# Performance work log

Measured on AMD Instinct MI355X. Metric: run time of the kernel, lower is better.

The kernel has to match this reference:

```python
import jax, jax.numpy as jnp
import numpy as np

N_NODES = 50000
N_EDGES = 800000
IN_DIM = 128
HID_DIM = 256
OUT_DIM = 5
BATCH = 50000  # batch_size in module; view(batch_size, 5)


def _sage_conv(x, src, dst, Wl, bl, Wr):
    # PyG SAGEConv (aggr='mean', root_weight=True, normalize=False):
    #   out = lin_l(mean_{j in N(i)} x_j) + lin_r(x_i)
    msgs = x[src]                                            # [E, d]
    agg = jax.ops.segment_sum(msgs, dst, num_segments=N_NODES)
    cnt = jax.ops.segment_sum(jnp.ones((src.shape[0],), x.dtype), dst,
                              num_segments=N_NODES)          # [N]
    mean = agg / jnp.maximum(cnt, 1.0)[:, None]              # 0 for isolated nodes
    return mean @ Wl.T + bl + x @ Wr.T


def setup_inputs() -> dict:
    key = jax.random.key(0)
    ks = jax.random.split(key, 8)
    x = jax.random.normal(ks[0], (N_NODES, IN_DIM), dtype=jnp.float32)
    edge_index = jax.random.randint(ks[1], (2, N_EDGES), 0, N_NODES, dtype=jnp.int64)
    s1 = 1.0 / np.sqrt(IN_DIM)
    s2 = 1.0 / np.sqrt(HID_DIM)
    W1l = jax.random.uniform(ks[2], (HID_DIM, IN_DIM), jnp.float32, -s1, s1)
    b1l = jax.random.uniform(ks[3], (HID_DIM,), jnp.float32, -s1, s1)
    W1r = jax.random.uniform(ks[4], (HID_DIM, IN_DIM), jnp.float32, -s1, s1)
    W2l = jax.random.uniform(ks[5], (OUT_DIM, HID_DIM), jnp.float32, -s2, s2)
    b2l = jax.random.uniform(ks[6], (OUT_DIM,), jnp.float32, -s2, s2)
    W2r = jax.random.uniform(ks[7], (OUT_DIM, HID_DIM), jnp.float32, -s2, s2)
    return {"x": x, "edge_index": edge_index,
            "W1l": W1l, "b1l": b1l, "W1r": W1r,
            "W2l": W2l, "b2l": b2l, "W2r": W2r}


def reference(x, edge_index, W1l, b1l, W1r, W2l, b2l, W2r):
    src, dst = edge_index[0], edge_index[1]
    h = jax.nn.relu(_sage_conv(x, src, dst, W1l, b1l, W1r))   # [N, hidden]
    h = jax.nn.relu(_sage_conv(h, src, dst, W2l, b2l, W2r))   # [N, out]
    return h.reshape(BATCH, 5)
```

## Files before the change

kernel.cpp:

```cpp
#include <hip/hip_runtime.h>

static constexpr int NN = 50000;
static constexpr int NE = 800000;
static constexpr int D0 = 128;
static constexpr int D1 = 256;
static constexpr int D2 = 5;

static constexpr int BSZ   = 256;
static constexpr int NBUK  = (NN + BSZ - 1) / BSZ;
static constexpr int CAP   = 4800;
static constexpr int CB    = 400;
static constexpr int CHUNK = 2000;

static constexpr int XB = (NN * 32 + 255) / 256;
static constexpr int WB = (D1 * 64) / 256;
static constexpr int PB = 4;

using short8  = __attribute__((ext_vector_type(8))) short;
using floatx4 = __attribute__((ext_vector_type(4))) float;

__device__ __forceinline__ unsigned short f2b(float f) {
  union { float f; unsigned u; } v; v.f = f;
  unsigned r = v.u + 0x7fffu + ((v.u >> 16) & 1u);
  return (unsigned short)(r >> 16);
}
__device__ __forceinline__ float b2f(unsigned short s) {
  union { unsigned u; float f; } v; v.u = ((unsigned)s) << 16;
  return v.f;
}

__global__ __launch_bounds__(256) void k_prepA(
    const float* __restrict__ x, unsigned short* __restrict__ ab,
    const float* __restrict__ W1l, const float* __restrict__ W1r,
    unsigned short* __restrict__ wb, const float* __restrict__ W2l,
    const float* __restrict__ W2r, unsigned short* __restrict__ w2b,
    const int* __restrict__ src, const int* __restrict__ dst,
    int* __restrict__ gcur, uint2* __restrict__ slab) {
  __shared__ int hist[256], bstart[256], gbase[256], hcur[256], sscan[256];
  __shared__ uint2 pairs[CHUNK];
  const int b = blockIdx.x, t = threadIdx.x;
  if (b < CB) {
    const int e0 = b * CHUNK;
    hist[t] = 0;
    __syncthreads();
    for (int j = t; j < CHUNK; j += 256)
      atomicAdd(&hist[dst[e0 + j] >> 8], 1);
    __syncthreads();
    sscan[t] = hist[t];
    __syncthreads();
    for (int dd = 1; dd < 256; dd <<= 1) {
      int u = (t >= dd) ? sscan[t - dd] : 0;
      __syncthreads();
      sscan[t] += u;
      __syncthreads();
    }
    bstart[t] = sscan[t] - hist[t];
    gbase[t] = (t < NBUK && hist[t] > 0) ? atomicAdd(&gcur[t], hist[t]) : 0;
    hcur[t] = 0;
    __syncthreads();
    for (int j = t; j < CHUNK; j += 256) {
      const int s = src[e0 + j], d = dst[e0 + j];
      const int bk = d >> 8;
      const int pos = bstart[bk] + atomicAdd(&hcur[bk], 1);
      pairs[pos] = make_uint2((unsigned)s, (unsigned)d);
    }
    __syncthreads();
    for (int j = t; j < CHUNK; j += 256) {
      const uint2 pr = pairs[j];
      const int bk = (int)pr.y >> 8;
      slab[(size_t)bk * CAP + gbase[bk] + (j - bstart[bk])] = pr;
    }
    return;
  }
  if (b < CB + XB) {
    int idx = (b - CB) * 256 + t;
    if (idx < NN * 32) {
      int node = idx >> 5, cg = idx & 31;
      float4 v = *(const float4*)(x + (size_t)node * D0 + cg * 4);
      ushort4 o;
      o.x = f2b(v.x); o.y = f2b(v.y); o.z = f2b(v.z); o.w = f2b(v.w);
      *(ushort4*)(ab + (size_t)node * 256 + 128 + cg * 4) = o;
    }
    return;
  }
  if (b < CB + XB + WB) {
    int idx = (b - CB - XB) * 256 + t;
    int c = idx >> 6, k = (idx & 63) * 4;
    const float* srcp = (k < 128) ? (W1l + (size_t)c * 128 + k)
                                  : (W1r + (size_t)c * 128 + (k - 128));
    float4 v = *(const float4*)srcp;
    ushort4 o;
    o.x = f2b(v.x); o.y = f2b(v.y); o.z = f2b(v.z); o.w = f2b(v.w);
    *(ushort4*)(wb + (size_t)c * 256 + k) = o;
    return;
  }
  {
    int idx = (b - CB - XB - WB) * 256 + t;
    int n = idx >> 6, k = (idx & 63) * 4;
    float4 v = {0.f, 0.f, 0.f, 0.f};
    if (n < 5) v = *(const float4*)(W2l + (size_t)n * D1 + k);
    else if (n < 10) v = *(const float4*)(W2r + (size_t)(n - 5) * D1 + k);
    ushort4 o;
    o.x = f2b(v.x); o.y = f2b(v.y); o.z = f2b(v.z); o.w = f2b(v.w);
    *(ushort4*)(w2b + (size_t)n * 256 + k) = o;
  }
}

__global__ __launch_bounds__(256) void k_bucketBC(
    const uint2* __restrict__ slab, const int* __restrict__ gcur,
    int* __restrict__ cur, float* __restrict__ inv,
    int* __restrict__ esort) {
  __shared__ int cnt[BSZ], s[BSZ], lcur[BSZ], g[256];
  __shared__ int sorted[CAP];
  const int b = blockIdx.x, t = threadIdx.x;
  const int n0 = b << 8;
  cnt[t] = 0;
  g[t] = (t < NBUK) ? gcur[t] : 0;
  __syncthreads();
  for (int dd = 1; dd < 256; dd <<= 1) {
    int u = (t >= dd) ? g[t - dd] : 0;
    __syncthreads();
    g[t] += u;
    __syncthreads();
  }
  const int bbase = (b == 0) ? 0 : g[b - 1];
  const int cntE = gcur[b];
  const uint2* sp = slab + (size_t)b * CAP;
  for (int j = t; j < cntE; j += 256)
    atomicAdd(&cnt[(int)sp[j].y - n0], 1);
  __syncthreads();
  s[t] = cnt[t];
  __syncthreads();
  for (int dd = 1; dd < BSZ; dd <<= 1) {
    int u = (t >= dd) ? s[t - dd] : 0;
    __syncthreads();
    s[t] += u;
    __syncthreads();
  }
  const int start = bbase + (s[t] - cnt[t]);
  const int node = n0 + t;
  if (node < NN) {
    cur[node] = start;
    inv[node] = 1.0f / (float)max(cnt[t], 1);
  }
  lcur[t] = s[t] - cnt[t];
  if (b == NBUK - 1 && t == 0) cur[NN] = NE;
  __syncthreads();
  for (int j = t; j < cntE; j += 256) {
    const uint2 pr = sp[j];
    const int p = atomicAdd(&lcur[(int)pr.y - n0], 1);
    sorted[p] = (int)pr.x;
  }
  __syncthreads();
  for (int j = t; j < cntE; j += 256)
    esort[bbase + j] = sorted[j];
}

__global__ __launch_bounds__(256) void k_agg1(
    unsigned short* __restrict__ ab, const int* __restrict__ esort,
    const int* __restrict__ cur, const float* __restrict__ inv) {
  const int i = (blockIdx.x * 256 + threadIdx.x) >> 6;
  const int lane = threadIdx.x & 63;
  if (i >= NN) return;
  int e = cur[i];
  const int end = cur[i + 1];
  float a0 = 0.f, b0 = 0.f, a1 = 0.f, b1 = 0.f;
  float a2 = 0.f, b2 = 0.f, a3 = 0.f, b3 = 0.f;
  const unsigned short* xb = ab + 128 + lane * 2;
  while (e < end && (e & 3)) {
    const unsigned v = *(const unsigned*)(xb + (size_t)esort[e] * 256);
    a0 += b2f((unsigned short)v); b0 += b2f((unsigned short)(v >> 16));
    ++e;
  }
  for (; e + 7 < end; e += 8) {
    const int4 s0 = *(const int4*)(esort + e);
    const int4 s1 = *(const int4*)(esort + e + 4);
    const unsigned v0 = *(const unsigned*)(xb + (size_t)s0.x * 256);
    const unsigned v1 = *(const unsigned*)(xb + (size_t)s0.y * 256);
    const unsigned v2 = *(const unsigned*)(xb + (size_t)s0.z * 256);
    const unsigned v3 = *(const unsigned*)(xb + (size_t)s0.w * 256);
    const unsigned v4 = *(const unsigned*)(xb + (size_t)s1.x * 256);
    const unsigned v5 = *(const unsigned*)(xb + (size_t)s1.y * 256);
    const unsigned v6 = *(const unsigned*)(xb + (size_t)s1.z * 256);
    const unsigned v7 = *(const unsigned*)(xb + (size_t)s1.w * 256);
    a0 += b2f((unsigned short)v0); b0 += b2f((unsigned short)(v0 >> 16));
    a1 += b2f((unsigned short)v1); b1 += b2f((unsigned short)(v1 >> 16));
    a2 += b2f((unsigned short)v2); b2 += b2f((unsigned short)(v2 >> 16));
    a3 += b2f((unsigned short)v3); b3 += b2f((unsigned short)(v3 >> 16));
    a0 += b2f((unsigned short)v4); b0 += b2f((unsigned short)(v4 >> 16));
    a1 += b2f((unsigned short)v5); b1 += b2f((unsigned short)(v5 >> 16));
    a2 += b2f((unsigned short)v6); b2 += b2f((unsigned short)(v6 >> 16));
    a3 += b2f((unsigned short)v7); b3 += b2f((unsigned short)(v7 >> 16));
  }
  if (e + 3 < end) {
    const int4 s0 = *(const int4*)(esort + e);
    const unsigned v0 = *(const unsigned*)(xb + (size_t)s0.x * 256);
    const unsigned v1 = *(const unsigned*)(xb + (size_t)s0.y * 256);
    const unsigned v2 = *(const unsigned*)(xb + (size_t)s0.z * 256);
    const unsigned v3 = *(const unsigned*)(xb + (size_t)s0.w * 256);
    a0 += b2f((unsigned short)v0); b0 += b2f((unsigned short)(v0 >> 16));
    a1 += b2f((unsigned short)v1); b1 += b2f((unsigned short)(v1 >> 16));
    a2 += b2f((unsigned short)v2); b2 += b2f((unsigned short)(v2 >> 16));
    a3 += b2f((unsigned short)v3); b3 += b2f((unsigned short)(v3 >> 16));
    e += 4;
  }
  for (; e < end; ++e) {
    const unsigned v = *(const unsigned*)(xb + (size_t)esort[e] * 256);
    a0 += b2f((unsigned short)v); b0 += b2f((unsigned short)(v >> 16));
  }
  const float sc = inv[i];
  const float sa = (a0 + a1) + (a2 + a3);
  const float sb = (b0 + b1) + (b2 + b3);
  const unsigned out =
      ((unsigned)f2b(sb * sc) << 16) | (unsigned)f2b(sa * sc);
  *(unsigned*)(ab + (size_t)i * 256 + lane * 2) = out;
}

__global__ __launch_bounds__(256) void k_gemm1f(
    const unsigned short* __restrict__ ab, const unsigned short* __restrict__ wb,
    const unsigned short* __restrict__ w2b, const float* __restrict__ b1l,
    float* __restrict__ tt, float* __restrict__ rp) {
  __shared__ short sAB[2 * 128 * 72];
  short* sA = sAB;
  short* sB = sAB + 128 * 72;
  const int tid = threadIdx.x;
  const int row0 = blockIdx.y * 128;
  const int hf = blockIdx.x;
  const int col0 = hf * 128;
  const int wave = tid >> 6, lane = tid & 63;
  const int quad = lane >> 4, m16 = lane & 15;
  const int wm = wave & 1, wn = wave >> 1;
  const int lr = tid >> 2;
  const int lk = (tid & 3) * 8;

  floatx4 acc[4][4];
#pragma unroll
  for (int a = 0; a < 4; ++a)
#pragma unroll
    for (int b = 0; b < 4; ++b) acc[a][b] = {0.f, 0.f, 0.f, 0.f};

  const int gr0 = row0 + lr, gr1 = row0 + lr + 64;
  const bool ok0 = gr0 < NN, ok1 = gr1 < NN;
  const unsigned short* aptr0 = ab + (size_t)gr0 * 256 + lk;
  const unsigned short* aptr1 = ab + (size_t)gr1 * 256 + lk;
  const unsigned short* bptr0 = wb + (size_t)(col0 + lr) * 256 + lk;
  const unsigned short* bptr1 = wb + (size_t)(col0 + lr + 64) * 256 + lk;
  short* sA0 = &sA[lr * 72 + lk];
  short* sA1 = &sA[(lr + 64) * 72 + lk];
  short* sB0 = &sB[lr * 72 + lk];
  short* sB1 = &sB[(lr + 64) * 72 + lk];
  const uint4 zz = make_uint4(0, 0, 0, 0);

  uint4 a00 = ok0 ? *(const uint4*)(aptr0) : zz;
  uint4 a01 = ok0 ? *(const uint4*)(aptr0 + 32) : zz;
  uint4 a10 = ok1 ? *(const uint4*)(aptr1) : zz;
  uint4 a11 = ok1 ? *(const uint4*)(aptr1 + 32) : zz;
  uint4 b00 = *(const uint4*)(bptr0);
  uint4 b01 = *(const uint4*)(bptr0 + 32);
  uint4 b10 = *(const uint4*)(bptr1);
  uint4 b11 = *(const uint4*)(bptr1 + 32);

  for (int kk = 0; kk < 256; kk += 64) {
    __syncthreads();
    *(uint4*)sA0 = a00;
    *(uint4*)(sA0 + 32) = a01;
    *(uint4*)sA1 = a10;
    *(uint4*)(sA1 + 32) = a11;
    *(uint4*)sB0 = b00;
    *(uint4*)(sB0 + 32) = b01;
    *(uint4*)sB1 = b10;
    *(uint4*)(sB1 + 32) = b11;
    __syncthreads();
    if (kk < 192) {
      const int kn = kk + 64;
      a00 = ok0 ? *(const uint4*)(aptr0 + kn) : zz;
      a01 = ok0 ? *(const uint4*)(aptr0 + kn + 32) : zz;
      a10 = ok1 ? *(const uint4*)(aptr1 + kn) : zz;
      a11 = ok1 ? *(const uint4*)(aptr1 + kn + 32) : zz;
      b00 = *(const uint4*)(bptr0 + kn);
      b01 = *(const uint4*)(bptr0 + kn + 32);
      b10 = *(const uint4*)(bptr1 + kn);
      b11 = *(const uint4*)(bptr1 + kn + 32);
    }
#pragma unroll
    for (int ko = 0; ko < 64; ko += 32) {
      short8 af[4], bf[4];
#pragma unroll
      for (int mt = 0; mt < 4; ++mt)
        af[mt] =
            *(const short8*)&sA[(wm * 64 + mt * 16 + m16) * 72 + ko + quad * 8];
#pragma unroll
      for (int nt = 0; nt < 4; ++nt)
        bf[nt] =
            *(const short8*)&sB[(wn * 64 + nt * 16 + m16) * 72 + ko + quad * 8];
#pragma unroll
      for (int mt = 0; mt < 4; ++mt)
#pragma unroll
        for (int nt = 0; nt < 4; ++nt)
          acc[mt][nt] = __builtin_amdgcn_mfma_f32_16x16x32_bf16(
              af[mt], bf[nt], acc[mt][nt], 0, 0, 0);
    }
  }

  __syncthreads();
  short* sH = sAB;
#pragma unroll
  for (int nt = 0; nt < 4; ++nt) {
    const int cl = wn * 64 + nt * 16 + m16;
    const float bias = b1l[col0 + cl];
#pragma unroll
    for (int mt = 0; mt < 4; ++mt)
#pragma unroll
      for (int rg = 0; rg < 4; ++rg) {
        const int rl = wm * 64 + mt * 16 + quad * 4 + rg;
        sH[rl * 136 + cl] = (short)f2b(fmaxf(acc[mt][nt][rg] + bias, 0.f));
      }
  }
  __syncthreads();
  floatx4 c2[2] = {{0.f, 0.f, 0.f, 0.f}, {0.f, 0.f, 0.f, 0.f}};
#pragma unroll
  for (int kb = 0; kb < 4; ++kb) {
    const short8 bf2 =
        *(const short8*)&w2b[m16 * 256 + col0 + kb * 32 + quad * 8];
#pragma unroll
    for (int i = 0; i < 2; ++i) {
      const int mrow = (wave * 2 + i) * 16 + m16;
      const short8 af2 = *(const short8*)&sH[mrow * 136 + kb * 32 + quad * 8];
      c2[i] = __builtin_amdgcn_mfma_f32_16x16x32_bf16(af2, bf2, c2[i], 0, 0, 0);
    }
  }
#pragma unroll
  for (int i = 0; i < 2; ++i) {
    const int rbase = row0 + (wave * 2 + i) * 16 + quad * 4;
#pragma unroll
    for (int rg = 0; rg < 4; ++rg) {
      const int row = rbase + rg;
      if (row < NN) {
        if (m16 < 5)
          tt[(size_t)row * 16 + hf * 8 + m16] = c2[i][rg];
        else if (m16 < 10)
          rp[(size_t)hf * ((size_t)NN * 8) + (size_t)row * 8 + (m16 - 5)] =
              c2[i][rg];
      }
    }
  }
}

__global__ __launch_bounds__(256) void k_layer2(
    const float* __restrict__ tt, const float* __restrict__ rp,
    const int* __restrict__ esort, const int* __restrict__ cur,
    const float* __restrict__ inv, const float* __restrict__ b2l,
    float* __restrict__ out) {
  const int node = blockIdx.x * 16 + (threadIdx.x >> 4);
  const int l = threadIdx.x & 15;
  if (node >= NN) return;
  const int beg = cur[node], end = cur[node + 1];
  float s = 0.f, u = 0.f;
  int e = beg;
  for (; e + 3 < end; e += 4) {
    const int4 r4 = *(const int4*)(esort + e);
    const float t0 = tt[(size_t)r4.x * 16 + l];
    const float t1 = tt[(size_t)r4.y * 16 + l];
    const float t2 = tt[(size_t)r4.z * 16 + l];
    const float t3 = tt[(size_t)r4.w * 16 + l];
    s += t0 + t2;
    u += t1 + t3;
  }
  for (; e < end; ++e) s += tt[(size_t)esort[e] * 16 + l];
  s += u;
  s += __shfl_xor(s, 8, 64);
  if (l < 5) {
    const float r = rp[(size_t)node * 8 + l] +
                    rp[(size_t)NN * 8 + (size_t)node * 8 + l];
    out[(size_t)node * D2 + l] = fmaxf(s * inv[node] + b2l[l] + r, 0.f);
  }
}

extern "C" void kernel_launch(void* const* d_in, const int* in_sizes, int n_in,
                              void* d_out, int out_size, void* d_ws,
                              size_t ws_size, hipStream_t stream) {
  const float* x   = (const float*)d_in[0];
  const int*   ei  = (const int*)d_in[1];
  const int*   src = ei;
  const int*   dst = ei + NE;
  const float* W1l = (const float*)d_in[2];
  const float* b1l = (const float*)d_in[3];
  const float* W1r = (const float*)d_in[4];
  const float* W2l = (const float*)d_in[5];
  const float* b2l = (const float*)d_in[6];
  const float* W2r = (const float*)d_in[7];
  float* out = (float*)d_out;

  unsigned short* ab  = (unsigned short*)d_ws;
  unsigned short* wb  = ab + (size_t)NN * 256;
  unsigned short* w2b = wb + 256 * 256;
  float* tt   = (float*)(w2b + 16 * 256);
  float* rp   = tt + (size_t)NN * 16;
  uint2* slab = (uint2*)(rp + (size_t)NN * 16);
  int*   gcur = (int*)(slab + (size_t)NBUK * CAP);
  int*   esort = gcur + 256;
  int*   cur  = esort + NE;
  float* inv  = (float*)(cur + NN + 4);

  hipMemsetAsync(gcur, 0, 256 * sizeof(int), stream);

  k_prepA<<<CB + XB + WB + PB, 256, 0, stream>>>(x, ab, W1l, W1r, wb, W2l, W2r,
                                                 w2b, src, dst, gcur, slab);
  k_bucketBC<<<NBUK, 256, 0, stream>>>(slab, gcur, cur, inv, esort);
  k_agg1<<<(NN * 64 + 255) / 256, 256, 0, stream>>>(ab, esort, cur, inv);
  dim3 g1(2, (NN + 127) / 128);
  k_gemm1f<<<g1, 256, 0, stream>>>(ab, wb, w2b, b1l, tt, rp);
  k_layer2<<<(NN + 15) / 16, 256, 0, stream>>>(tt, rp, esort, cur, inv, b2l,
                                               out);
}
```

Measured before the change: 177.8 us.

## Fuse mean aggregation into layer-1 GEMM kernel with shared A tile

The separate neighbor-aggregation kernel is merged into the GEMM kernel. Each 512-thread block first aggregates its own 128 rows, writing them to global memory, then syncs and runs two 256-thread groups that each compute one 128-column half of the output. The A tile is loaded once into shared memory and shared by both halves, which removes a kernel launch and the duplicate A reads. In exchange there are fewer blocks (391) with larger LDS use, which may reduce the latency hiding available to the irregular gather phase.

Measured after the change: 252.8 us. +42.2%, slower.

```diff
diff --git a/kernel.cpp b/kernel.cpp
--- a/kernel.cpp
+++ b/kernel.cpp
@@ -156,82 +156,88 @@
     esort[bbase + j] = sorted[j];
 }
 
-__global__ __launch_bounds__(256) void k_agg1(
-    unsigned short* __restrict__ ab, const int* __restrict__ esort,
-    const int* __restrict__ cur, const float* __restrict__ inv) {
-  const int i = (blockIdx.x * 256 + threadIdx.x) >> 6;
-  const int lane = threadIdx.x & 63;
-  if (i >= NN) return;
-  int e = cur[i];
-  const int end = cur[i + 1];
-  float a0 = 0.f, b0 = 0.f, a1 = 0.f, b1 = 0.f;
-  float a2 = 0.f, b2 = 0.f, a3 = 0.f, b3 = 0.f;
-  const unsigned short* xb = ab + 128 + lane * 2;
-  while (e < end && (e & 3)) {
-    const unsigned v = *(const unsigned*)(xb + (size_t)esort[e] * 256);
-    a0 += b2f((unsigned short)v); b0 += b2f((unsigned short)(v >> 16));
-    ++e;
-  }
-  for (; e + 7 < end; e += 8) {
-    const int4 s0 = *(const int4*)(esort + e);
-    const int4 s1 = *(const int4*)(esort + e + 4);
-    const unsigned v0 = *(const unsigned*)(xb + (size_t)s0.x * 256);
-    const unsigned v1 = *(const unsigned*)(xb + (size_t)s0.y * 256);
-    const unsigned v2 = *(const unsigned*)(xb + (size_t)s0.z * 256);
-    const unsigned v3 = *(const unsigned*)(xb + (size_t)s0.w * 256);
-    const unsigned v4 = *(const unsigned*)(xb + (size_t)s1.x * 256);
-    const unsigned v5 = *(const unsigned*)(xb + (size_t)s1.y * 256);
-    const unsigned v6 = *(const unsigned*)(xb + (size_t)s1.z * 256);
-    const unsigned v7 = *(const unsigned*)(xb + (size_t)s1.w * 256);
-    a0 += b2f((unsigned short)v0); b0 += b2f((unsigned short)(v0 >> 16));
-    a1 += b2f((unsigned short)v1); b1 += b2f((unsigned short)(v1 >> 16));
-    a2 += b2f((unsigned short)v2); b2 += b2f((unsigned short)(v2 >> 16));
-    a3 += b2f((unsigned short)v3); b3 += b2f((unsigned short)(v3 >> 16));
-    a0 += b2f((unsigned short)v4); b0 += b2f((unsigned short)(v4 >> 16));
-    a1 += b2f((unsigned short)v5); b1 += b2f((unsigned short)(v5 >> 16));
-    a2 += b2f((unsigned short)v6); b2 += b2f((unsigned short)(v6 >> 16));
-    a3 += b2f((unsigned short)v7); b3 += b2f((unsigned short)(v7 >> 16));
-  }
-  if (e + 3 < end) {
-    const int4 s0 = *(const int4*)(esort + e);
-    const unsigned v0 = *(const unsigned*)(xb + (size_t)s0.x * 256);
-    const unsigned v1 = *(const unsigned*)(xb + (size_t)s0.y * 256);
-    const unsigned v2 = *(const unsigned*)(xb + (size_t)s0.z * 256);
-    const unsigned v3 = *(const unsigned*)(xb + (size_t)s0.w * 256);
-    a0 += b2f((unsigned short)v0); b0 += b2f((unsigned short)(v0 >> 16));
-    a1 += b2f((unsigned short)v1); b1 += b2f((unsigned short)(v1 >> 16));
-    a2 += b2f((unsigned short)v2); b2 += b2f((unsigned short)(v2 >> 16));
-    a3 += b2f((unsigned short)v3); b3 += b2f((unsigned short)(v3 >> 16));
-    e += 4;
-  }
-  for (; e < end; ++e) {
-    const unsigned v = *(const unsigned*)(xb + (size_t)esort[e] * 256);
-    a0 += b2f((unsigned short)v); b0 += b2f((unsigned short)(v >> 16));
-  }
-  const float sc = inv[i];
-  const float sa = (a0 + a1) + (a2 + a3);
-  const float sb = (b0 + b1) + (b2 + b3);
-  const unsigned out =
-      ((unsigned)f2b(sb * sc) << 16) | (unsigned)f2b(sa * sc);
-  *(unsigned*)(ab + (size_t)i * 256 + lane * 2) = out;
-}
-
-__global__ __launch_bounds__(256) void k_gemm1f(
-    const unsigned short* __restrict__ ab, const unsigned short* __restrict__ wb,
+__global__ __launch_bounds__(512) void k_aggemm(
+    unsigned short* __restrict__ ab, const unsigned short* __restrict__ wb,
     const unsigned short* __restrict__ w2b, const float* __restrict__ b1l,
-    float* __restrict__ tt, float* __restrict__ rp) {
-  __shared__ short sAB[2 * 128 * 72];
-  short* sA = sAB;
-  short* sB = sAB + 128 * 72;
+    const int* __restrict__ esort, const int* __restrict__ cur,
+    const float* __restrict__ inv, float* __restrict__ tt,
+    float* __restrict__ rp) {
+  __shared__ short smem[2 * 128 * 136];
+  const int row0 = blockIdx.x * 128;
   const int tid = threadIdx.x;
-  const int row0 = blockIdx.y * 128;
-  const int hf = blockIdx.x;
-  const int col0 = hf * 128;
-  const int wave = tid >> 6, lane = tid & 63;
+
+  {
+    const int wv = tid >> 6;
+    const int lane = tid & 63;
+    const unsigned short* xb = ab + 128 + lane * 2;
+    for (int it = 0; it < 16; ++it) {
+      const int i = row0 + it * 8 + wv;
+      if (i >= NN) break;
+      int e = cur[i];
+      const int end = cur[i + 1];
+      float a0 = 0.f, b0 = 0.f, a1 = 0.f, b1 = 0.f;
+      float a2 = 0.f, b2 = 0.f, a3 = 0.f, b3 = 0.f;
+      while (e < end && (e & 3)) {
+        const unsigned v = *(const unsigned*)(xb + (size_t)esort[e] * 256);
+        a0 += b2f((unsigned short)v); b0 += b2f((unsigned short)(v >> 16));
+        ++e;
+      }
+      for (; e + 7 < end; e += 8) {
+        const int4 s0 = *(const int4*)(esort + e);
+        const int4 s1 = *(const int4*)(esort + e + 4);
+        const unsigned v0 = *(const unsigned*)(xb + (size_t)s0.x * 256);
+        const unsigned v1 = *(const unsigned*)(xb + (size_t)s0.y * 256);
+        const unsigned v2 = *(const unsigned*)(xb + (size_t)s0.z * 256);
+        const unsigned v3 = *(const unsigned*)(xb + (size_t)s0.w * 256);
+        const unsigned v4 = *(const unsigned*)(xb + (size_t)s1.x * 256);
+        const unsigned v5 = *(const unsigned*)(xb + (size_t)s1.y * 256);
+        const unsigned v6 = *(const unsigned*)(xb + (size_t)s1.z * 256);
+        const unsigned v7 = *(const unsigned*)(xb + (size_t)s1.w * 256);
+        a0 += b2f((unsigned short)v0); b0 += b2f((unsigned short)(v0 >> 16));
+        a1 += b2f((unsigned short)v1); b1 += b2f((unsigned short)(v1 >> 16));
+        a2 += b2f((unsigned short)v2); b2 += b2f((unsigned short)(v2 >> 16));
+        a3 += b2f((unsigned short)v3); b3 += b2f((unsigned short)(v3 >> 16));
+        a0 += b2f((unsigned short)v4); b0 += b2f((unsigned short)(v4 >> 16));
+        a1 += b2f((unsigned short)v5); b1 += b2f((unsigned short)(v5 >> 16));
+        a2 += b2f((unsigned short)v6); b2 += b2f((unsigned short)(v6 >> 16));
+        a3 += b2f((unsigned short)v7); b3 += b2f((unsigned short)(v7 >> 16));
+      }
+      if (e + 3 < end) {
+        const int4 s0 = *(const int4*)(esort + e);
+        const unsigned v0 = *(const unsigned*)(xb + (size_t)s0.x * 256);
+        const unsigned v1 = *(const unsigned*)(xb + (size_t)s0.y * 256);
+        const unsigned v2 = *(const unsigned*)(xb + (size_t)s0.z * 256);
+        const unsigned v3 = *(const unsigned*)(xb + (size_t)s0.w * 256);
+        a0 += b2f((unsigned short)v0); b0 += b2f((unsigned short)(v0 >> 16));
+        a1 += b2f((unsigned short)v1); b1 += b2f((unsigned short)(v1 >> 16));
+        a2 += b2f((unsigned short)v2); b2 += b2f((unsigned short)(v2 >> 16));
+        a3 += b2f((unsigned short)v3); b3 += b2f((unsigned short)(v3 >> 16));
+        e += 4;
+      }
+      for (; e < end; ++e) {
+        const unsigned v = *(const unsigned*)(xb + (size_t)esort[e] * 256);
+        a0 += b2f((unsigned short)v); b0 += b2f((unsigned short)(v >> 16));
+      }
+      const float sc = inv[i];
+      const float sa = (a0 + a1) + (a2 + a3);
+      const float sb = (b0 + b1) + (b2 + b3);
+      const unsigned o =
+          ((unsigned)f2b(sb * sc) << 16) | (unsigned)f2b(sa * sc);
+      *(unsigned*)(ab + (size_t)i * 256 + lane * 2) = o;
+    }
+  }
+  __syncthreads();
+
+  const int g = tid >> 8;
+  const int tid8 = tid & 255;
+  short* sA = smem;
+  short* sB = smem + (1 + g) * (128 * 72);
+  const int wave = tid8 >> 6, lane = tid8 & 63;
   const int quad = lane >> 4, m16 = lane & 15;
   const int wm = wave & 1, wn = wave >> 1;
-  const int lr = tid >> 2;
-  const int lk = (tid & 3) * 8;
+  const int lr = tid8 >> 2;
+  const int lk = (tid8 & 3) * 8;
+  const int col0 = g * 128;
 
   floatx4 acc[4][4];
 #pragma unroll
@@ -251,10 +257,13 @@
   short* sB1 = &sB[(lr + 64) * 72 + lk];
   const uint4 zz = make_uint4(0, 0, 0, 0);
 
-  uint4 a00 = ok0 ? *(const uint4*)(aptr0) : zz;
-  uint4 a01 = ok0 ? *(const uint4*)(aptr0 + 32) : zz;
-  uint4 a10 = ok1 ? *(const uint4*)(aptr1) : zz;
-  uint4 a11 = ok1 ? *(const uint4*)(aptr1 + 32) : zz;
+  uint4 a00 = zz, a01 = zz, a10 = zz, a11 = zz;
+  if (g == 0) {
+    a00 = ok0 ? *(const uint4*)(aptr0) : zz;
+    a01 = ok0 ? *(const uint4*)(aptr0 + 32) : zz;
+    a10 = ok1 ? *(const uint4*)(aptr1) : zz;
+    a11 = ok1 ? *(const uint4*)(aptr1 + 32) : zz;
+  }
   uint4 b00 = *(const uint4*)(bptr0);
   uint4 b01 = *(const uint4*)(bptr0 + 32);
   uint4 b10 = *(const uint4*)(bptr1);
@@ -262,10 +271,12 @@
 
   for (int kk = 0; kk < 256; kk += 64) {
     __syncthreads();
-    *(uint4*)sA0 = a00;
-    *(uint4*)(sA0 + 32) = a01;
-    *(uint4*)sA1 = a10;
-    *(uint4*)(sA1 + 32) = a11;
+    if (g == 0) {
+      *(uint4*)sA0 = a00;
+      *(uint4*)(sA0 + 32) = a01;
+      *(uint4*)sA1 = a10;
+      *(uint4*)(sA1 + 32) = a11;
+    }
     *(uint4*)sB0 = b00;
     *(uint4*)(sB0 + 32) = b01;
     *(uint4*)sB1 = b10;
@@ -273,10 +284,12 @@
     __syncthreads();
     if (kk < 192) {
       const int kn = kk + 64;
-      a00 = ok0 ? *(const uint4*)(aptr0 + kn) : zz;
-      a01 = ok0 ? *(const uint4*)(aptr0 + kn + 32) : zz;
-      a10 = ok1 ? *(const uint4*)(aptr1 + kn) : zz;
-      a11 = ok1 ? *(const uint4*)(aptr1 + kn + 32) : zz;
+      if (g == 0) {
+        a00 = ok0 ? *(const uint4*)(aptr0 + kn) : zz;
+        a01 = ok0 ? *(const uint4*)(aptr0 + kn + 32) : zz;
+        a10 = ok1 ? *(const uint4*)(aptr1 + kn) : zz;
+        a11 = ok1 ? *(const uint4*)(aptr1 + kn + 32) : zz;
+      }
       b00 = *(const uint4*)(bptr0 + kn);
       b01 = *(const uint4*)(bptr0 + kn + 32);
       b10 = *(const uint4*)(bptr1 + kn);
@@ -303,7 +316,7 @@
   }
 
   __syncthreads();
-  short* sH = sAB;
+  short* sH = smem + g * (128 * 136);
 #pragma unroll
   for (int nt = 0; nt < 4; ++nt) {
     const int cl = wn * 64 + nt * 16 + m16;
@@ -337,9 +350,9 @@
       const int row = rbase + rg;
       if (row < NN) {
         if (m16 < 5)
-          tt[(size_t)row * 16 + hf * 8 + m16] = c2[i][rg];
+          tt[(size_t)row * 16 + g * 8 + m16] = c2[i][rg];
         else if (m16 < 10)
-          rp[(size_t)hf * ((size_t)NN * 8) + (size_t)row * 8 + (m16 - 5)] =
+          rp[(size_t)g * ((size_t)NN * 8) + (size_t)row * 8 + (m16 - 5)] =
               c2[i][rg];
       }
     }
@@ -407,9 +420,8 @@
   k_prepA<<<CB + XB + WB + PB, 256, 0, stream>>>(x, ab, W1l, W1r, wb, W2l, W2r,
                                                  w2b, src, dst, gcur, slab);
   k_bucketBC<<<NBUK, 256, 0, stream>>>(slab, gcur, cur, inv, esort);
-  k_agg1<<<(NN * 64 + 255) / 256, 256, 0, stream>>>(ab, esort, cur, inv);
-  dim3 g1(2, (NN + 127) / 128);
-  k_gemm1f<<<g1, 256, 0, stream>>>(ab, wb, w2b, b1l, tt, rp);
+  k_aggemm<<<(NN + 127) / 128, 512, 0, stream>>>(ab, wb, w2b, b1l, esort, cur,
+                                                 inv, tt, rp);
   k_layer2<<<(NN + 15) / 16, 256, 0, stream>>>(tt, rp, esort, cur, inv, b2l,
                                                out);
 }
```

## Fuse aggregation and layer-1 GEMM into one kernel with per-tile completion counters

Applied to the files above, without the earlier changes.

Merges the neighbor-mean aggregation kernel and the fused layer-1/layer-2-projection GEMM kernel into a single launch. Aggregation blocks bump a per-128-row-tile counter after writing. GEMM blocks spin on that counter before loading their tile, so GEMM work can start while other tiles are still aggregating and one launch boundary disappears. The cost is spin-wait overhead and a reliance on aggregation blocks being scheduled before the GEMM blocks that wait on them. Aggregation blocks now also carry the GEMM's shared-memory allocation, which may lower their occupancy.

Result: slower. 605.0 us (+240.3%).

```diff
diff --git a/kernel.cpp b/kernel.cpp
--- a/kernel.cpp
+++ b/kernel.cpp
@@ -15,6 +15,10 @@
 static constexpr int XB = (NN * 32 + 255) / 256;
 static constexpr int WB = (D1 * 64) / 256;
 static constexpr int PB = 4;
+
+static constexpr int AGB = NN / 4;
+static constexpr int NT  = (NN + 127) / 128;
+static constexpr int GMB = 2 * NT;
 
 using short8  = __attribute__((ext_vector_type(8))) short;
 using floatx4 = __attribute__((ext_vector_type(4))) float;
@@ -156,77 +160,97 @@
     esort[bbase + j] = sorted[j];
 }
 
-__global__ __launch_bounds__(256) void k_agg1(
-    unsigned short* __restrict__ ab, const int* __restrict__ esort,
-    const int* __restrict__ cur, const float* __restrict__ inv) {
-  const int i = (blockIdx.x * 256 + threadIdx.x) >> 6;
-  const int lane = threadIdx.x & 63;
-  if (i >= NN) return;
-  int e = cur[i];
-  const int end = cur[i + 1];
-  float a0 = 0.f, b0 = 0.f, a1 = 0.f, b1 = 0.f;
-  float a2 = 0.f, b2 = 0.f, a3 = 0.f, b3 = 0.f;
-  const unsigned short* xb = ab + 128 + lane * 2;
-  while (e < end && (e & 3)) {
-    const unsigned v = *(const unsigned*)(xb + (size_t)esort[e] * 256);
-    a0 += b2f((unsigned short)v); b0 += b2f((unsigned short)(v >> 16));
-    ++e;
-  }
-  for (; e + 7 < end; e += 8) {
-    const int4 s0 = *(const int4*)(esort + e);
-    const int4 s1 = *(const int4*)(esort + e + 4);
-    const unsigned v0 = *(const unsigned*)(xb + (size_t)s0.x * 256);
-    const unsigned v1 = *(const unsigned*)(xb + (size_t)s0.y * 256);
-    const unsigned v2 = *(const unsigned*)(xb + (size_t)s0.z * 256);
-    const unsigned v3 = *(const unsigned*)(xb + (size_t)s0.w * 256);
-    const unsigned v4 = *(const unsigned*)(xb + (size_t)s1.x * 256);
-    const unsigned v5 = *(const unsigned*)(xb + (size_t)s1.y * 256);
-    const unsigned v6 = *(const unsigned*)(xb + (size_t)s1.z * 256);
-    const unsigned v7 = *(const unsigned*)(xb + (size_t)s1.w * 256);
-    a0 += b2f((unsigned short)v0); b0 += b2f((unsigned short)(v0 >> 16));
-    a1 += b2f((unsigned short)v1); b1 += b2f((unsigned short)(v1 >> 16));
-    a2 += b2f((unsigned short)v2); b2 += b2f((unsigned short)(v2 >> 16));
-    a3 += b2f((unsigned short)v3); b3 += b2f((unsigned short)(v3 >> 16));
-    a0 += b2f((unsigned short)v4); b0 += b2f((unsigned short)(v4 >> 16));
-    a1 += b2f((unsigned short)v5); b1 += b2f((unsigned short)(v5 >> 16));
-    a2 += b2f((unsigned short)v6); b2 += b2f((unsigned short)(v6 >> 16));
-    a3 += b2f((unsigned short)v7); b3 += b2f((unsigned short)(v7 >> 16));
-  }
-  if (e + 3 < end) {
-    const int4 s0 = *(const int4*)(esort + e);
-    const unsigned v0 = *(const unsigned*)(xb + (size_t)s0.x * 256);
-    const unsigned v1 = *(const unsigned*)(xb + (size_t)s0.y * 256);
-    const unsigned v2 = *(const unsigned*)(xb + (size_t)s0.z * 256);
-    const unsigned v3 = *(const unsigned*)(xb + (size_t)s0.w * 256);
-    a0 += b2f((unsigned short)v0); b0 += b2f((unsigned short)(v0 >> 16));
-    a1 += b2f((unsigned short)v1); b1 += b2f((unsigned short)(v1 >> 16));
-    a2 += b2f((unsigned short)v2); b2 += b2f((unsigned short)(v2 >> 16));
-    a3 += b2f((unsigned short)v3); b3 += b2f((unsigned short)(v3 >> 16));
-    e += 4;
-  }
-  for (; e < end; ++e) {
-    const unsigned v = *(const unsigned*)(xb + (size_t)esort[e] * 256);
-    a0 += b2f((unsigned short)v); b0 += b2f((unsigned short)(v >> 16));
-  }
-  const float sc = inv[i];
-  const float sa = (a0 + a1) + (a2 + a3);
-  const float sb = (b0 + b1) + (b2 + b3);
-  const unsigned out =
-      ((unsigned)f2b(sb * sc) << 16) | (unsigned)f2b(sa * sc);
-  *(unsigned*)(ab + (size_t)i * 256 + lane * 2) = out;
-}
-
-__global__ __launch_bounds__(256) void k_gemm1f(
-    const unsigned short* __restrict__ ab, const unsigned short* __restrict__ wb,
+__global__ __launch_bounds__(256) void k_aggemm2(
+    unsigned short* __restrict__ ab, const unsigned short* __restrict__ wb,
     const unsigned short* __restrict__ w2b, const float* __restrict__ b1l,
-    float* __restrict__ tt, float* __restrict__ rp) {
+    const int* __restrict__ esort, const int* __restrict__ cur,
+    const float* __restrict__ inv, float* __restrict__ tt,
+    float* __restrict__ rp, int* __restrict__ done) {
   __shared__ short sAB[2 * 128 * 72];
+  const int blk = blockIdx.x;
+  const int tid = threadIdx.x;
+
+  if (blk < AGB) {
+    const int i = blk * 4 + (tid >> 6);
+    const int lane = tid & 63;
+    int e = cur[i];
+    const int end = cur[i + 1];
+    float a0 = 0.f, b0 = 0.f, a1 = 0.f, b1 = 0.f;
+    float a2 = 0.f, b2 = 0.f, a3 = 0.f, b3 = 0.f;
+    const unsigned short* xb = ab + 128 + lane * 2;
+    while (e < end && (e & 3)) {
+      const unsigned v = *(const unsigned*)(xb + (size_t)esort[e] * 256);
+      a0 += b2f((unsigned short)v); b0 += b2f((unsigned short)(v >> 16));
+      ++e;
+    }
+    for (; e + 7 < end; e += 8) {
+      const int4 s0 = *(const int4*)(esort + e);
+      const int4 s1 = *(const int4*)(esort + e + 4);
+      const unsigned v0 = *(const unsigned*)(xb + (size_t)s0.x * 256);
+      const unsigned v1 = *(const unsigned*)(xb + (size_t)s0.y * 256);
+      const unsigned v2 = *(const unsigned*)(xb + (size_t)s0.z * 256);
+      const unsigned v3 = *(const unsigned*)(xb + (size_t)s0.w * 256);
+      const unsigned v4 = *(const unsigned*)(xb + (size_t)s1.x * 256);
+      const unsigned v5 = *(const unsigned*)(xb + (size_t)s1.y * 256);
+      const unsigned v6 = *(const unsigned*)(xb + (size_t)s1.z * 256);
+      const unsigned v7 = *(const unsigned*)(xb + (size_t)s1.w * 256);
+      a0 += b2f((unsigned short)v0); b0 += b2f((unsigned short)(v0 >> 16));
+      a1 += b2f((unsigned short)v1); b1 += b2f((unsigned short)(v1 >> 16));
+      a2 += b2f((unsigned short)v2); b2 += b2f((unsigned short)(v2 >> 16));
+      a3 += b2f((unsigned short)v3); b3 += b2f((unsigned short)(v3 >> 16));
+      a0 += b2f((unsigned short)v4); b0 += b2f((unsigned short)(v4 >> 16));
+      a1 += b2f((unsigned short)v5); b1 += b2f((unsigned short)(v5 >> 16));
+      a2 += b2f((unsigned short)v6); b2 += b2f((unsigned short)(v6 >> 16));
+      a3 += b2f((unsigned short)v7); b3 += b2f((unsigned short)(v7 >> 16));
+    }
+    if (e + 3 < end) {
+      const int4 s0 = *(const int4*)(esort + e);
+      const unsigned v0 = *(const unsigned*)(xb + (size_t)s0.x * 256);
+      const unsigned v1 = *(const unsigned*)(xb + (size_t)s0.y * 256);
+      const unsigned v2 = *(const unsigned*)(xb + (size_t)s0.z * 256);
+      const unsigned v3 = *(const unsigned*)(xb + (size_t)s0.w * 256);
+      a0 += b2f((unsigned short)v0); b0 += b2f((unsigned short)(v0 >> 16));
+      a1 += b2f((unsigned short)v1); b1 += b2f((unsigned short)(v1 >> 16));
+      a2 += b2f((unsigned short)v2); b2 += b2f((unsigned short)(v2 >> 16));
+      a3 += b2f((unsigned short)v3); b3 += b2f((unsigned short)(v3 >> 16));
+      e += 4;
+    }
+    for (; e < end; ++e) {
+      const unsigned v = *(const unsigned*)(xb + (size_t)esort[e] * 256);
+      a0 += b2f((unsigned short)v); b0 += b2f((unsigned short)(v >> 16));
+    }
+    const float sc = inv[i];
+    const float sa = (a0 + a1) + (a2 + a3);
+    const float sb = (b0 + b1) + (b2 + b3);
+    const unsigned o =
+        ((unsigned)f2b(sb * sc) << 16) | (unsigned)f2b(sa * sc);
+    *(unsigned*)(ab + (size_t)i * 256 + lane * 2) = o;
+    __syncthreads();
+    if (tid == 0) {
+      __threadfence();
+      __hip_atomic_fetch_add(done + (blk >> 5), 1, __ATOMIC_RELAXED,
+                             __HIP_MEMORY_SCOPE_AGENT);
+    }
+    return;
+  }
+
+  const int cid = blk - AGB;
+  const int t = cid >> 1;
+  const int g = cid & 1;
+  const int row0 = t * 128;
+  const int col0 = g * 128;
+  const int expected = min(32, (NN - row0 + 3) >> 2);
+
+  if (tid == 0) {
+    while (__hip_atomic_load(done + t, __ATOMIC_RELAXED,
+                             __HIP_MEMORY_SCOPE_AGENT) < expected)
+      __builtin_amdgcn_s_sleep(2);
+  }
+  __syncthreads();
+  __threadfence();
+
   short* sA = sAB;
   short* sB = sAB + 128 * 72;
-  const int tid = threadIdx.x;
-  const int row0 = blockIdx.y * 128;
-  const int hf = blockIdx.x;
-  const int col0 = hf * 128;
   const int wave = tid >> 6, lane = tid & 63;
   const int quad = lane >> 4, m16 = lane & 15;
   const int wm = wave & 1, wn = wave >> 1;
@@ -337,9 +361,9 @@
       const int row = rbase + rg;
       if (row < NN) {
         if (m16 < 5)
-          tt[(size_t)row * 16 + hf * 8 + m16] = c2[i][rg];
+          tt[(size_t)row * 16 + g * 8 + m16] = c2[i][rg];
         else if (m16 < 10)
-          rp[(size_t)hf * ((size_t)NN * 8) + (size_t)row * 8 + (m16 - 5)] =
+          rp[(size_t)g * ((size_t)NN * 8) + (size_t)row * 8 + (m16 - 5)] =
               c2[i][rg];
       }
     }
@@ -398,18 +422,18 @@
   float* rp   = tt + (size_t)NN * 16;
   uint2* slab = (uint2*)(rp + (size_t)NN * 16);
   int*   gcur = (int*)(slab + (size_t)NBUK * CAP);
-  int*   esort = gcur + 256;
+  int*   done = gcur + 256;
+  int*   esort = gcur + 768;
   int*   cur  = esort + NE;
   float* inv  = (float*)(cur + NN + 4);
 
-  hipMemsetAsync(gcur, 0, 256 * sizeof(int), stream);
+  hipMemsetAsync(gcur, 0, 768 * sizeof(int), stream);
 
   k_prepA<<<CB + XB + WB + PB, 256, 0, stream>>>(x, ab, W1l, W1r, wb, W2l, W2r,
                                                  w2b, src, dst, gcur, slab);
   k_bucketBC<<<NBUK, 256, 0, stream>>>(slab, gcur, cur, inv, esort);
-  k_agg1<<<(NN * 64 + 255) / 256, 256, 0, stream>>>(ab, esort, cur, inv);
-  dim3 g1(2, (NN + 127) / 128);
-  k_gemm1f<<<g1, 256, 0, stream>>>(ab, wb, w2b, b1l, tt, rp);
+  k_aggemm2<<<AGB + GMB, 256, 0, stream>>>(ab, wb, w2b, b1l, esort, cur, inv,
+                                           tt, rp, done);
   k_layer2<<<(NN + 15) / 16, 256, 0, stream>>>(tt, rp, esort, cur, inv, b2l,
                                                out);
 }
```
